# Optimization experiments

Hardware: AMD Instinct MI355X
Metric: run time of the kernel (lower is better)

## Reference

```python
import jax, jax.numpy as jnp
import numpy as np

EPS = 1e-6
INV_T = 1.0
STEPS = 4
S = 1  # MD_S
R = 1  # MD_R


def setup_inputs() -> dict:
    key = jax.random.key(0)
    k1, k2 = jax.random.split(key)
    # NMF operates on non-negative data -> uniform [0,1)
    x = jax.random.uniform(k1, (4, 16, 160, 72, 72), dtype=jnp.float32)
    bases = jax.random.uniform(k2, (4 * S, 160 // S, R), dtype=jnp.float32)
    # _build_bases: F.normalize(bases, dim=1) -> L2 normalize over D axis
    bases = bases / jnp.maximum(jnp.linalg.norm(bases, axis=1, keepdims=True), 1e-12)
    return {"x": x, "bases": bases}


def _local_step(xr, bases, coef):
    # xr: [B, D, N], bases: [B, D, R], coef: [B, N, R]
    # multiplicative NMF update for coef
    num_c = jnp.einsum('bdn,bdr->bnr', xr, bases)                     # x^T b
    btb = jnp.einsum('bdr,bds->brs', bases, bases)                    # b^T b  [B,R,R]
    coef = coef * num_c / (jnp.einsum('bnr,brs->bns', coef, btb) + EPS)
    # multiplicative NMF update for bases
    num_b = jnp.einsum('bdn,bnr->bdr', xr, coef)                      # x c
    ctc = jnp.einsum('bnr,bns->brs', coef, coef)                      # c^T c  [B,R,R]
    bases = bases * num_b / (jnp.einsum('bdr,brs->bds', bases, ctc) + EPS)
    return bases, coef


def _compute_coef(xr, bases, coef):
    num_c = jnp.einsum('bdn,bdr->bnr', xr, bases)
    btb = jnp.einsum('bdr,bds->brs', bases, bases)
    return coef * num_c / (jnp.einsum('bnr,brs->bns', coef, btb) + EPS)


def reference(x, bases):
    B, C, T, H, W = x.shape
    D = T // S
    N = C * H * W
    xr = x.reshape(B * S, D, N)  # [4, 160, 82944]

    def local_inference(xr, bases):
        coef = jax.nn.softmax(INV_T * jnp.einsum('bdn,bdr->bnr', xr, bases), axis=-1)
        for _ in range(STEPS):
            bases, coef = _local_step(xr, bases, coef)
        return bases, coef

    # local_inference is @torch.no_grad() in the original
    bases_f, coef = jax.lax.stop_gradient(local_inference(xr, bases))
    coef = _compute_coef(xr, bases_f, coef)
    out = jnp.einsum('bdr,bnr->bdn', bases_f, coef)  # bases @ coef^T
    return out.reshape(B, C, T, H, W)
```

## Files before the change

kernel.cpp:

```cpp
#include <hip/hip_runtime.h>
#include <hip/hip_bf16.h>

#define EPS 1e-6f

constexpr int D  = 160;
constexpr int NN = 82944;
constexpr int B  = 4;

typedef __bf16 bf16x8 __attribute__((ext_vector_type(8)));
typedef __bf16 bf16x4 __attribute__((ext_vector_type(4)));
typedef float  floatx4 __attribute__((ext_vector_type(4)));

constexpr int BK = 64;
constexpr int BKP = BK + 8;
constexpr int SLABS = 8;
constexpr int COLS_PER_BLOCK = BK * SLABS;
constexpr int GRAM_BLOCKS = NN / COLS_PER_BLOCK;

__global__ __launch_bounds__(256, 2)
void gram_kernel(const float* __restrict__ x, float* __restrict__ P)
{
    __shared__ __align__(16) __bf16 xs[2][D * BKP];

    const int tid = threadIdx.x;
    const int batch = blockIdx.y;
    const int w  = tid >> 6;
    const int l  = tid & 63;
    const int lr = l & 15;
    const int lq = l >> 4;
    const int itile0 = (w & 1) * 5;
    const int jtile0 = (w >> 1) * 5;
    const int srow = tid >> 4;
    const int scol = (tid & 15) * 4;

    const float* xb = x + (size_t)batch * D * NN + (size_t)blockIdx.x * COLS_PER_BLOCK;
    const float* pbase = xb + (size_t)srow * NN + scol;

    floatx4 acc[5][5] = {};
    float4 pf[10];

    #pragma unroll
    for (int p = 0; p < 10; ++p)
        pf[p] = *(const float4*)(pbase + (size_t)p * 16 * NN);

    for (int s = 0; s < SLABS; ++s) {
        __bf16* buf = xs[s & 1];
        #pragma unroll
        for (int p = 0; p < 10; ++p) {
            bf16x4 h = { (__bf16)pf[p].x, (__bf16)pf[p].y, (__bf16)pf[p].z, (__bf16)pf[p].w };
            *(bf16x4*)&buf[(srow + p * 16) * BKP + scol] = h;
        }
        if (s + 1 < SLABS) {
            const float* pn = pbase + (s + 1) * BK;
            #pragma unroll
            for (int p = 0; p < 10; ++p)
                pf[p] = *(const float4*)(pn + (size_t)p * 16 * NN);
        }
        __syncthreads();
        #pragma unroll
        for (int k = 0; k < BK / 32; ++k) {
            bf16x8 fa[5], fb[5];
            #pragma unroll
            for (int i = 0; i < 5; ++i) {
                fa[i] = *(const bf16x8*)&buf[((itile0 + i) * 16 + lr) * BKP + k * 32 + lq * 8];
                fb[i] = *(const bf16x8*)&buf[((jtile0 + i) * 16 + lr) * BKP + k * 32 + lq * 8];
            }
            #pragma unroll
            for (int i = 0; i < 5; ++i)
                #pragma unroll
                for (int j = 0; j < 5; ++j)
                    acc[i][j] = __builtin_amdgcn_mfma_f32_16x16x32_bf16(fa[i], fb[j], acc[i][j], 0, 0, 0);
        }
    }

    float* Pb = P + ((size_t)batch * GRAM_BLOCKS + blockIdx.x) * (size_t)(D * D)
                  + w * 6400 + l * 4;
    #pragma unroll
    for (int i = 0; i < 5; ++i)
        #pragma unroll
        for (int j = 0; j < 5; ++j)
            __builtin_nontemporal_store(acc[i][j], (floatx4*)(Pb + (i * 5 + j) * 256));
}

__global__ __launch_bounds__(256)
void reduce_kernel(const float* __restrict__ P, float* __restrict__ G)
{
    const int batch = blockIdx.y;
    const int f4 = (blockIdx.x * 256 + threadIdx.x) * 4;
    const float* p = P + (size_t)batch * GRAM_BLOCKS * D * D + f4;
    floatx4 s = {0.f, 0.f, 0.f, 0.f};
    #pragma unroll 9
    for (int k = 0; k < GRAM_BLOCKS; ++k)
        s += __builtin_nontemporal_load((const floatx4*)(p + (size_t)k * D * D));

    const int w   = f4 / 6400;
    const int rem = f4 % 6400;
    const int t   = rem / 256;
    const int q   = rem % 256;
    const int i   = t / 5;
    const int j   = t % 5;
    const int l   = q >> 2;
    const int d1b = (w & 1) * 80 + i * 16 + (l >> 4) * 4;
    const int d2  = (w >> 1) * 80 + j * 16 + (l & 15);
    float* Gb = G + (size_t)batch * D * D;
    #pragma unroll
    for (int r = 0; r < 4; ++r)
        Gb[(size_t)(d1b + r) * D + d2] = s[r];
}

__device__ __forceinline__ float block_reduce_bcast(float v, float* red)
{
    #pragma unroll
    for (int off = 32; off > 0; off >>= 1)
        v += __shfl_xor(v, off, 64);
    const int w = threadIdx.x >> 6;
    if ((threadIdx.x & 63) == 0) red[w] = v;
    __syncthreads();
    float s = red[0] + red[1] + red[2] + red[3];
    __syncthreads();
    return s;
}

__global__ __launch_bounds__(256)
void iter_kernel(const float* __restrict__ bases, const float* __restrict__ G,
                 float* __restrict__ bvec, float* __restrict__ svec)
{
    __shared__ float bs[D];
    __shared__ float red[4];
    const int batch = blockIdx.x;
    const int tid = threadIdx.x;
    const float* Gb = G + (size_t)batch * D * D;

    if (tid < D) bs[tid] = bases[batch * D + tid];
    __syncthreads();

    for (int step = 0; step < 4; ++step) {
        float v = (tid < D) ? bs[tid] * bs[tid] : 0.0f;
        const float btb = block_reduce_bcast(v, red);
        const float gamma = btb + EPS;

        float m = 0.0f;
        if (tid < D) {
            const float* row = Gb + (size_t)tid * D;
            #pragma unroll 8
            for (int j = 0; j < D; j += 4) {
                float4 g4 = *(const float4*)(row + j);
                m += g4.x * bs[j] + g4.y * bs[j + 1] + g4.z * bs[j + 2] + g4.w * bs[j + 3];
            }
        }
        float bm = (tid < D) ? bs[tid] * m : 0.0f;
        const float beta = block_reduce_bcast(bm, red);
        const float ctc = beta / (gamma * gamma);

        __syncthreads();
        if (tid < D) {
            const float bd = bs[tid];
            bs[tid] = bd * (m / gamma) / (bd * ctc + EPS);
        }
        __syncthreads();
    }

    float v = (tid < D) ? bs[tid] * bs[tid] : 0.0f;
    const float btb = block_reduce_bcast(v, red);
    const float inv = 1.0f / (btb + EPS);
    if (tid < D) {
        bvec[batch * D + tid] = bs[tid];
        svec[batch * D + tid] = bs[tid] * inv;
    }
}

__global__ __launch_bounds__(256)
void out_kernel(const float* __restrict__ x, const float* __restrict__ bvec,
                const float* __restrict__ svec, float* __restrict__ out)
{
    __shared__ float bsh[D], ssh[D];
    __shared__ floatx4 partA[256];
    __shared__ floatx4 partB[256];

    const int tid = threadIdx.x;
    const int batch = blockIdx.y;
    const int g = tid >> 5;
    const int lane = tid & 31;
    const size_t base0 = (size_t)batch * D * NN + (size_t)blockIdx.x * 256 + lane * 4;
    const size_t base1 = base0 + 128;

    if (tid < D) { bsh[tid] = bvec[batch * D + tid]; ssh[tid] = svec[batch * D + tid]; }
    __syncthreads();

    floatx4 t0 = {0.f, 0.f, 0.f, 0.f};
    floatx4 t1 = {0.f, 0.f, 0.f, 0.f};
    #pragma unroll
    for (int d = g; d < D; d += 8) {
        floatx4 xv0 = *(const floatx4*)(x + base0 + (size_t)d * NN);
        floatx4 xv1 = *(const floatx4*)(x + base1 + (size_t)d * NN);
        const float bd = bsh[d];
        t0 += xv0 * bd;
        t1 += xv1 * bd;
    }
    partA[tid] = t0;
    partB[tid] = t1;
    __syncthreads();
    if (tid < 32) {
        floatx4 s = partA[tid];
        #pragma unroll
        for (int k = 1; k < 8; ++k) s += partA[k * 32 + tid];
        partA[tid] = s;
    } else if (tid < 64) {
        floatx4 s = partB[tid - 32];
        #pragma unroll
        for (int k = 1; k < 8; ++k) s += partB[k * 32 + (tid - 32)];
        partB[tid - 32] = s;
    }
    __syncthreads();
    t0 = partA[lane];
    t1 = partB[lane];

    #pragma unroll
    for (int d = g; d < D; d += 8) {
        const float sd = ssh[d];
        floatx4 o0 = t0 * sd;
        floatx4 o1 = t1 * sd;
        __builtin_nontemporal_store(o0, (floatx4*)(out + base0 + (size_t)d * NN));
        __builtin_nontemporal_store(o1, (floatx4*)(out + base1 + (size_t)d * NN));
    }
}

extern "C" void kernel_launch(void* const* d_in, const int* in_sizes, int n_in,
                              void* d_out, int out_size, void* d_ws, size_t ws_size,
                              hipStream_t stream)
{
    (void)in_sizes; (void)n_in; (void)out_size; (void)ws_size;
    const float* x     = (const float*)d_in[0];
    const float* bases = (const float*)d_in[1];
    float* out = (float*)d_out;

    float* P    = (float*)d_out;
    float* G    = (float*)d_out + (size_t)50000000;
    float* bvec = (float*)d_ws;
    float* svec = bvec + B * D;

    gram_kernel<<<dim3(GRAM_BLOCKS, B), 256, 0, stream>>>(x, P);
    reduce_kernel<<<dim3(25, B), 256, 0, stream>>>(P, G);
    iter_kernel<<<dim3(B), 256, 0, stream>>>(bases, G, bvec, svec);
    out_kernel<<<dim3(NN / 256, B), 256, 0, stream>>>(x, bvec, svec, out);
}
```

Measured before the change: 440.3 us.

## Load Gram slabs via global_load_lds with swizzle, simplify output kernel

New measurement: 440.2 us. No clear change (-0.0%).

```diff
diff --git a/kernel.cpp b/kernel.cpp
--- a/kernel.cpp
+++ b/kernel.cpp
@@ -8,19 +8,22 @@
 constexpr int B  = 4;
 
 typedef __bf16 bf16x8 __attribute__((ext_vector_type(8)));
-typedef __bf16 bf16x4 __attribute__((ext_vector_type(4)));
 typedef float  floatx4 __attribute__((ext_vector_type(4)));
 
 constexpr int BK = 64;
-constexpr int BKP = BK + 8;
-constexpr int SLABS = 8;
+constexpr int SLABS = 16;
 constexpr int COLS_PER_BLOCK = BK * SLABS;
 constexpr int GRAM_BLOCKS = NN / COLS_PER_BLOCK;
 
+#define GLD16(gp, lp)                                                               \
+    __builtin_amdgcn_global_load_lds(                                               \
+        (const __attribute__((address_space(1))) unsigned int*)(const void*)(gp),   \
+        (__attribute__((address_space(3))) unsigned int*)(void*)(lp), 16, 0, 0)
+
 __global__ __launch_bounds__(256, 2)
 void gram_kernel(const float* __restrict__ x, float* __restrict__ P)
 {
-    __shared__ __align__(16) __bf16 xs[2][D * BKP];
+    __shared__ __align__(16) float xs[2][D * BK];
 
     const int tid = threadIdx.x;
     const int batch = blockIdx.y;
@@ -28,50 +31,75 @@
     const int l  = tid & 63;
     const int lr = l & 15;
     const int lq = l >> 4;
+    const int lr7 = lr & 7;
     const int itile0 = (w & 1) * 5;
     const int jtile0 = (w >> 1) * 5;
-    const int srow = tid >> 4;
-    const int scol = (tid & 15) * 4;
+
+    const int rbase = w * 40 + (l >> 4);
+    const int jg0   = (l & 15) ^ (l >> 4);
 
     const float* xb = x + (size_t)batch * D * NN + (size_t)blockIdx.x * COLS_PER_BLOCK;
-    const float* pbase = xb + (size_t)srow * NN + scol;
 
     floatx4 acc[5][5] = {};
-    float4 pf[10];
-
-    #pragma unroll
-    for (int p = 0; p < 10; ++p)
-        pf[p] = *(const float4*)(pbase + (size_t)p * 16 * NN);
-
-    for (int s = 0; s < SLABS; ++s) {
-        __bf16* buf = xs[s & 1];
-        #pragma unroll
-        for (int p = 0; p < 10; ++p) {
-            bf16x4 h = { (__bf16)pf[p].x, (__bf16)pf[p].y, (__bf16)pf[p].z, (__bf16)pf[p].w };
-            *(bf16x4*)&buf[(srow + p * 16) * BKP + scol] = h;
+
+    #define ISSUE_SLAB(SIDX, BUF) {                                                 \
+        const float* gs_ = xb + (size_t)(SIDX) * BK;                                \
+        _Pragma("unroll")                                                           \
+        for (int p = 0; p < 10; ++p) {                                              \
+            const int row_ = rbase + p * 4;                                         \
+            const int jg_  = jg0 ^ ((p & 1) << 2);                                  \
+            GLD16(gs_ + (size_t)row_ * NN + jg_ * 4,                                \
+                  &(BUF)[(w * 40 + p * 4) * BK]);                                   \
+        } }
+
+    #define FRAG_LOAD(TILE, F, BUFP) {                                              \
+        const float* rp_ = (BUFP) + ((TILE) * 16 + lr) * BK;                         \
+        const floatx4 va_ = *(const floatx4*)(rp_ + ((sbase ^ lr7) << 2));           \
+        const floatx4 vb_ = *(const floatx4*)(rp_ + (((sbase + 1) ^ lr7) << 2));     \
+        bf16x8 f_;                                                                   \
+        f_[0] = (__bf16)va_.x; f_[1] = (__bf16)va_.y;                                \
+        f_[2] = (__bf16)va_.z; f_[3] = (__bf16)va_.w;                                \
+        f_[4] = (__bf16)vb_.x; f_[5] = (__bf16)vb_.y;                                \
+        f_[6] = (__bf16)vb_.z; f_[7] = (__bf16)vb_.w;                                \
+        F = f_; }
+
+    #define COMPUTE_SLAB(BUF) {                                                     \
+        const float* bufp_ = (BUF);                                                  \
+        _Pragma("unroll")                                                            \
+        for (int kk = 0; kk < 2; ++kk) {                                             \
+            const int sbase = kk * 8 + lq * 2;                                       \
+            bf16x8 fa[5], fb[5];                                                     \
+            _Pragma("unroll")                                                        \
+            for (int i = 0; i < 5; ++i) {                                            \
+                FRAG_LOAD(itile0 + i, fa[i], bufp_);                                 \
+                FRAG_LOAD(jtile0 + i, fb[i], bufp_);                                 \
+            }                                                                        \
+            _Pragma("unroll")                                                        \
+            for (int i = 0; i < 5; ++i)                                              \
+                _Pragma("unroll")                                                    \
+                for (int j = 0; j < 5; ++j)                                          \
+                    acc[i][j] = __builtin_amdgcn_mfma_f32_16x16x32_bf16(             \
+                        fa[i], fb[j], acc[i][j], 0, 0, 0);                           \
+        } }
+
+    ISSUE_SLAB(0, xs[0]);
+
+    #pragma unroll 2
+    for (int k = 0; k < SLABS; ++k) {
+        float* bufk = xs[k & 1];
+        if (k + 1 < SLABS) {
+            ISSUE_SLAB(k + 1, xs[(k + 1) & 1]);
+            asm volatile("s_waitcnt vmcnt(10)" ::: "memory");
+        } else {
+            asm volatile("s_waitcnt vmcnt(0)" ::: "memory");
         }
-        if (s + 1 < SLABS) {
-            const float* pn = pbase + (s + 1) * BK;
-            #pragma unroll
-            for (int p = 0; p < 10; ++p)
-                pf[p] = *(const float4*)(pn + (size_t)p * 16 * NN);
-        }
-        __syncthreads();
-        #pragma unroll
-        for (int k = 0; k < BK / 32; ++k) {
-            bf16x8 fa[5], fb[5];
-            #pragma unroll
-            for (int i = 0; i < 5; ++i) {
-                fa[i] = *(const bf16x8*)&buf[((itile0 + i) * 16 + lr) * BKP + k * 32 + lq * 8];
-                fb[i] = *(const bf16x8*)&buf[((jtile0 + i) * 16 + lr) * BKP + k * 32 + lq * 8];
-            }
-            #pragma unroll
-            for (int i = 0; i < 5; ++i)
-                #pragma unroll
-                for (int j = 0; j < 5; ++j)
-                    acc[i][j] = __builtin_amdgcn_mfma_f32_16x16x32_bf16(fa[i], fb[j], acc[i][j], 0, 0, 0);
-        }
+        asm volatile("s_barrier" ::: "memory");
+        COMPUTE_SLAB(bufk);
+        asm volatile("s_barrier" ::: "memory");
     }
+    #undef ISSUE_SLAB
+    #undef FRAG_LOAD
+    #undef COMPUTE_SLAB
 
     float* Pb = P + ((size_t)batch * GRAM_BLOCKS + blockIdx.x) * (size_t)(D * D)
                   + w * 6400 + l * 4;
@@ -169,60 +197,24 @@
     }
 }
 
-__global__ __launch_bounds__(256)
+__global__ __launch_bounds__(64)
 void out_kernel(const float* __restrict__ x, const float* __restrict__ bvec,
                 const float* __restrict__ svec, float* __restrict__ out)
 {
-    __shared__ float bsh[D], ssh[D];
-    __shared__ floatx4 partA[256];
-    __shared__ floatx4 partB[256];
-
-    const int tid = threadIdx.x;
     const int batch = blockIdx.y;
-    const int g = tid >> 5;
-    const int lane = tid & 31;
-    const size_t base0 = (size_t)batch * D * NN + (size_t)blockIdx.x * 256 + lane * 4;
-    const size_t base1 = base0 + 128;
-
-    if (tid < D) { bsh[tid] = bvec[batch * D + tid]; ssh[tid] = svec[batch * D + tid]; }
-    __syncthreads();
-
-    floatx4 t0 = {0.f, 0.f, 0.f, 0.f};
-    floatx4 t1 = {0.f, 0.f, 0.f, 0.f};
-    #pragma unroll
-    for (int d = g; d < D; d += 8) {
-        floatx4 xv0 = *(const floatx4*)(x + base0 + (size_t)d * NN);
-        floatx4 xv1 = *(const floatx4*)(x + base1 + (size_t)d * NN);
-        const float bd = bsh[d];
-        t0 += xv0 * bd;
-        t1 += xv1 * bd;
-    }
-    partA[tid] = t0;
-    partB[tid] = t1;
-    __syncthreads();
-    if (tid < 32) {
-        floatx4 s = partA[tid];
-        #pragma unroll
-        for (int k = 1; k < 8; ++k) s += partA[k * 32 + tid];
-        partA[tid] = s;
-    } else if (tid < 64) {
-        floatx4 s = partB[tid - 32];
-        #pragma unroll
-        for (int k = 1; k < 8; ++k) s += partB[k * 32 + (tid - 32)];
-        partB[tid - 32] = s;
-    }
-    __syncthreads();
-    t0 = partA[lane];
-    t1 = partB[lane];
-
-    #pragma unroll
-    for (int d = g; d < D; d += 8) {
-        const float sd = ssh[d];
-        floatx4 o0 = t0 * sd;
-        floatx4 o1 = t1 * sd;
-        __builtin_nontemporal_store(o0, (floatx4*)(out + base0 + (size_t)d * NN));
-        __builtin_nontemporal_store(o1, (floatx4*)(out + base1 + (size_t)d * NN));
-    }
+    const size_t base = (size_t)batch * D * NN + (size_t)blockIdx.x * 256
+                      + ((size_t)threadIdx.x << 2);
+    const float* bb = bvec + batch * D;
+    const float* ss = svec + batch * D;
+
+    floatx4 t = {0.f, 0.f, 0.f, 0.f};
+    #pragma unroll 8
+    for (int d = 0; d < D; ++d)
+        t += *(const floatx4*)(x + base + (size_t)d * NN) * bb[d];
+
+    #pragma unroll 8
+    for (int d = 0; d < D; ++d)
+        __builtin_nontemporal_store(t * ss[d], (floatx4*)(out + base + (size_t)d * NN));
 }
 
 extern "C" void kernel_launch(void* const* d_in, const int* in_sizes, int n_in,
@@ -242,5 +234,5 @@
     gram_kernel<<<dim3(GRAM_BLOCKS, B), 256, 0, stream>>>(x, P);
     reduce_kernel<<<dim3(25, B), 256, 0, stream>>>(P, G);
     iter_kernel<<<dim3(B), 256, 0, stream>>>(bases, G, bvec, svec);
-    out_kernel<<<dim3(NN / 256, B), 256, 0, stream>>>(x, bvec, svec, out);
-}
+    out_kernel<<<dim3(NN / 256, B), 64, 0, stream>>>(x, bvec, svec, out);
+}
```
